# Optimization experiments

Hardware: AMD Instinct MI355X
Metric: run time of the kernel (lower is better)

Reference implementation:

```python
import jax, jax.numpy as jnp
import numpy as np


def setup_inputs() -> dict:
    key = jax.random.key(0)
    k_x, k_w = jax.random.split(key)
    H, W = 6144, 6144
    KH, KW = 7, 7
    x = jax.random.normal(k_x, (H, W), dtype=jnp.float32)
    weight = jax.random.uniform(k_w, (KH, KW), dtype=jnp.float32)
    bias = jnp.zeros((1,), dtype=jnp.float32)
    return {"x": x, "weight": weight, "bias": bias}


def reference(x, weight, bias):
    # Valid (no-padding) 2D cross-correlation, single channel.
    # x: [H, W], weight: [KH, KW] -> Y: [H-KH+1, W-KW+1] + bias
    lhs = x[None, None, :, :]            # [N=1, C=1, H, W]
    rhs = weight[None, None, :, :]       # [O=1, I=1, KH, KW]
    y = jax.lax.conv_general_dilated(
        lhs, rhs,
        window_strides=(1, 1),
        padding='VALID',
        dimension_numbers=('NCHW', 'OIHW', 'NCHW'),
    )
    return y[0, 0] + bias[0]
```

## Files before the change

### kernel.cpp

```cpp
#include <hip/hip_runtime.h>

#define H_IN 6144
#define W_IN 6144
#define KH 7
#define KW 7
#define H_OUT (H_IN - KH + 1)
#define W_OUT (W_IN - KW + 1)

#define TX 64
#define TY 32
#define RY 8
#define IN_W (TX + KW - 1)
#define IN_H (TY + KH - 1)
#define LDS_W 72
#define NV4 18
#define SHIFT_N (IN_H - TY)
#define SHIFT_ELT (SHIFT_N * LDS_W)

#define TILES_PER_BLK 4
#define GX 96
#define GYC 48
#define NWG (GX * GYC)
#define NXCD 8

__global__ __launch_bounds__(256, 4) void conv7x7_kernel(
    const float* __restrict__ x,
    const float* __restrict__ wgt,
    const float* __restrict__ bias,
    float* __restrict__ out)
{
    __shared__ float s[IN_H][LDS_W];

    const int tid = threadIdx.x;
    const int tx  = tid & 63;
    const int tq  = tid >> 6;

    const int bid = blockIdx.x;
    const int swz = (bid & (NXCD - 1)) * (NWG / NXCD) + (bid >> 3);
    const int bx  = swz % GX;
    const int byc = swz / GX;

    const int x0    = bx * TX;
    const int ybase = byc * (TY * TILES_PER_BLK);

    const float b = bias[0];

    auto stage = [&](int r0, int gy0) {
        const int nch = (IN_H - r0) * NV4;
        for (int idx = tid; idx < nch; idx += 256) {
            const int r  = r0 + idx / NV4;
            const int c  = idx % NV4;
            const int gy = gy0 + r;
            const int gx = x0 + (c << 2);
            float4 v = make_float4(0.f, 0.f, 0.f, 0.f);
            if (gy < H_IN) {
                if (gx + 3 < W_IN) {
                    v = *reinterpret_cast<const float4*>(&x[gy * W_IN + gx]);
                } else {
                    float t0 = (gx + 0 < W_IN) ? x[gy * W_IN + gx + 0] : 0.f;
                    float t1 = (gx + 1 < W_IN) ? x[gy * W_IN + gx + 1] : 0.f;
                    float t2 = (gx + 2 < W_IN) ? x[gy * W_IN + gx + 2] : 0.f;
                    float t3 = (gx + 3 < W_IN) ? x[gy * W_IN + gx + 3] : 0.f;
                    v = make_float4(t0, t1, t2, t3);
                }
            }
            *reinterpret_cast<float4*>(&s[r][c << 2]) = v;
        }
    };

    stage(0, ybase);
    __syncthreads();

    for (int t = 0; t < TILES_PER_BLK; ++t) {
        const int y0 = ybase + t * TY;

        float acc[RY];
#pragma unroll
        for (int r = 0; r < RY; ++r) acc[r] = 0.f;

        const int ry0 = tq * RY;

#pragma unroll
        for (int kx = 0; kx < KW; ++kx) {
            float v[RY + KH - 1];
#pragma unroll
            for (int j = 0; j < RY + KH - 1; ++j)
                v[j] = s[ry0 + j][tx + kx];
#pragma unroll
            for (int ky = 0; ky < KH; ++ky) {
                const float wv = wgt[ky * KW + kx];
#pragma unroll
                for (int r = 0; r < RY; ++r)
                    acc[r] = fmaf(wv, v[r + ky], acc[r]);
            }
        }

        const int ox = x0 + tx;
        if (ox < W_OUT) {
#pragma unroll
            for (int r = 0; r < RY; ++r) {
                const int oy = y0 + ry0 + r;
                if (oy < H_OUT) out[oy * W_OUT + ox] = acc[r] + b;
            }
        }

        if (t + 1 < TILES_PER_BLK) {
            const int i2 = tid + 256;
            float sh0 = s[TY + tid / LDS_W][tid % LDS_W];
            float sh1 = 0.f;
            if (i2 < SHIFT_ELT) sh1 = s[TY + i2 / LDS_W][i2 % LDS_W];
            __syncthreads();
            s[tid / LDS_W][tid % LDS_W] = sh0;
            if (i2 < SHIFT_ELT) s[i2 / LDS_W][i2 % LDS_W] = sh1;
            stage(SHIFT_N, y0 + TY);
            __syncthreads();
        }
    }
}

extern "C" void kernel_launch(void* const* d_in, const int* in_sizes, int n_in,
                              void* d_out, int out_size, void* d_ws, size_t ws_size,
                              hipStream_t stream) {
    const float* x    = (const float*)d_in[0];
    const float* wgt  = (const float*)d_in[1];
    const float* bias = (const float*)d_in[2];
    float* out        = (float*)d_out;

    conv7x7_kernel<<<dim3(NWG), dim3(256), 0, stream>>>(x, wgt, bias, out);
}
```

Baseline: 295.4 us.

## Use ring-buffered LDS and prefetch next tile rows into registers during compute

Replaces the per-tile LDS shift of halo rows with a 64-row circular buffer indexed modulo, so halo rows no longer need copying. The next tile's 32 new input rows are loaded from global memory into registers before the compute loop and written to LDS afterward, overlapping global load latency with FMA work. This costs extra registers (up to 3 float4) and slightly more LDS (64 rows instead of 38), which could lower occupancy.

```diff
diff --git a/kernel.cpp b/kernel.cpp
--- a/kernel.cpp
+++ b/kernel.cpp
@@ -14,8 +14,7 @@
 #define IN_H (TY + KH - 1)
 #define LDS_W 72
 #define NV4 18
-#define SHIFT_N (IN_H - TY)
-#define SHIFT_ELT (SHIFT_N * LDS_W)
+#define LDS_ROWS 64
 
 #define TILES_PER_BLK 4
 #define GX 96
@@ -23,13 +22,16 @@
 #define NWG (GX * GYC)
 #define NXCD 8
 
+#define CH_TILE (TY * NV4)
+#define MAXCH 3
+
 __global__ __launch_bounds__(256, 4) void conv7x7_kernel(
     const float* __restrict__ x,
     const float* __restrict__ wgt,
     const float* __restrict__ bias,
     float* __restrict__ out)
 {
-    __shared__ float s[IN_H][LDS_W];
+    __shared__ float s[LDS_ROWS][LDS_W];
 
     const int tid = threadIdx.x;
     const int tx  = tid & 63;
@@ -45,34 +47,47 @@
 
     const float b = bias[0];
 
-    auto stage = [&](int r0, int gy0) {
-        const int nch = (IN_H - r0) * NV4;
-        for (int idx = tid; idx < nch; idx += 256) {
-            const int r  = r0 + idx / NV4;
-            const int c  = idx % NV4;
-            const int gy = gy0 + r;
-            const int gx = x0 + (c << 2);
-            float4 v = make_float4(0.f, 0.f, 0.f, 0.f);
-            if (gy < H_IN) {
-                if (gx + 3 < W_IN) {
-                    v = *reinterpret_cast<const float4*>(&x[gy * W_IN + gx]);
-                } else {
-                    float t0 = (gx + 0 < W_IN) ? x[gy * W_IN + gx + 0] : 0.f;
-                    float t1 = (gx + 1 < W_IN) ? x[gy * W_IN + gx + 1] : 0.f;
-                    float t2 = (gx + 2 < W_IN) ? x[gy * W_IN + gx + 2] : 0.f;
-                    float t3 = (gx + 3 < W_IN) ? x[gy * W_IN + gx + 3] : 0.f;
-                    v = make_float4(t0, t1, t2, t3);
-                }
+    auto fetch = [&](int gy, int gx) -> float4 {
+        float4 v = make_float4(0.f, 0.f, 0.f, 0.f);
+        if (gy < H_IN) {
+            if (gx + 3 < W_IN) {
+                v = *reinterpret_cast<const float4*>(&x[gy * W_IN + gx]);
+            } else {
+                float t0 = (gx + 0 < W_IN) ? x[gy * W_IN + gx + 0] : 0.f;
+                float t1 = (gx + 1 < W_IN) ? x[gy * W_IN + gx + 1] : 0.f;
+                float t2 = (gx + 2 < W_IN) ? x[gy * W_IN + gx + 2] : 0.f;
+                float t3 = (gx + 3 < W_IN) ? x[gy * W_IN + gx + 3] : 0.f;
+                v = make_float4(t0, t1, t2, t3);
             }
-            *reinterpret_cast<float4*>(&s[r][c << 2]) = v;
         }
+        return v;
     };
 
-    stage(0, ybase);
+    for (int idx = tid; idx < IN_H * NV4; idx += 256) {
+        const int r = idx / NV4;
+        const int c = idx % NV4;
+        float4 v = fetch(ybase + r, x0 + (c << 2));
+        *reinterpret_cast<float4*>(&s[r][c << 2]) = v;
+    }
     __syncthreads();
 
     for (int t = 0; t < TILES_PER_BLK; ++t) {
         const int y0 = ybase + t * TY;
+        const int l0 = (t & 1) * TY;
+
+        float4 stg[MAXCH];
+        const bool do_stage = (t + 1 < TILES_PER_BLK);
+        if (do_stage) {
+#pragma unroll
+            for (int k = 0; k < MAXCH; ++k) {
+                const int idx = tid + (k << 8);
+                if (idx < CH_TILE) {
+                    const int r = idx / NV4;
+                    const int c = idx % NV4;
+                    stg[k] = fetch(y0 + IN_H + r, x0 + (c << 2));
+                }
+            }
+        }
 
         float acc[RY];
 #pragma unroll
@@ -85,7 +100,7 @@
             float v[RY + KH - 1];
 #pragma unroll
             for (int j = 0; j < RY + KH - 1; ++j)
-                v[j] = s[ry0 + j][tx + kx];
+                v[j] = s[(l0 + ry0 + j) & (LDS_ROWS - 1)][tx + kx];
 #pragma unroll
             for (int ky = 0; ky < KH; ++ky) {
                 const float wv = wgt[ky * KW + kx];
@@ -104,15 +119,18 @@
             }
         }
 
-        if (t + 1 < TILES_PER_BLK) {
-            const int i2 = tid + 256;
-            float sh0 = s[TY + tid / LDS_W][tid % LDS_W];
-            float sh1 = 0.f;
-            if (i2 < SHIFT_ELT) sh1 = s[TY + i2 / LDS_W][i2 % LDS_W];
+        if (do_stage) {
             __syncthreads();
-            s[tid / LDS_W][tid % LDS_W] = sh0;
-            if (i2 < SHIFT_ELT) s[i2 / LDS_W][i2 % LDS_W] = sh1;
-            stage(SHIFT_N, y0 + TY);
+#pragma unroll
+            for (int k = 0; k < MAXCH; ++k) {
+                const int idx = tid + (k << 8);
+                if (idx < CH_TILE) {
+                    const int r    = idx / NV4;
+                    const int c    = idx % NV4;
+                    const int slot = (l0 + IN_H + r) & (LDS_ROWS - 1);
+                    *reinterpret_cast<float4*>(&s[slot][c << 2]) = stg[k];
+                }
+            }
             __syncthreads();
         }
     }
```

After: 291.5 us. No clear change (-1.3%).
